# Kernel optimization log

Measured on AMD Instinct MI355X. Metric: run time of the kernel, lower is better.

The kernel has to match this reference:

```python
import jax, jax.numpy as jnp
import numpy as np

T_MAX = 20
NUM_HEADS = 8
COMPLEXITY_W = 0.3
LN_EPS = 1e-5


def _layernorm(h, g, b):
    mu = jnp.mean(h, axis=-1, keepdims=True)
    var = jnp.var(h, axis=-1, keepdims=True)
    return (h - mu) / jnp.sqrt(var + LN_EPS) * g + b


def _gate_mlp(x, W1, b1, g, be, W2, b2, W3, b3):
    # Linear -> LayerNorm -> ReLU -> (Dropout=id in eval) -> Linear -> ReLU -> Linear -> Sigmoid
    h = jax.nn.relu(_layernorm(x @ W1 + b1, g, be))
    h = jax.nn.relu(h @ W2 + b2)
    return jax.nn.sigmoid(h @ W3 + b3)


def _adaptive_windows(x, p):
    S = x.shape[1]
    gate = _gate_mlp(x, p['gW1'], p['gb1'], p['gg'], p['gbe'], p['gW2'], p['gb2'], p['gW3'], p['gb3'])
    comp = _gate_mlp(x, p['cW1'], p['cb1'], p['cg'], p['cbe'], p['cW2'], p['cb2'], p['cW3'], p['cb3'])
    pos = jnp.linspace(0.8, 1.2, S, dtype=x.dtype).reshape(1, -1, 1)
    score = ((1.0 - COMPLEXITY_W) * gate + COMPLEXITY_W * comp) * pos
    T_i = jnp.clip(jnp.ceil(score[..., 0] * T_MAX), 1, T_MAX).astype(jnp.int32)  # [B,S]
    return T_i


def _spike_sum(x, T_i, alpha, beta):
    # LIF recurrence over T_MAX steps; accumulate masked spikes. x: [B,S,E]
    z = jnp.zeros_like(x)

    def step(carry, t):
        v, i, acc = carry
        active = (t < T_i).astype(x.dtype)[..., None]  # [B,S,1]
        i = alpha * i + x * active
        v = beta * v + i
        s = (v >= 1.0).astype(x.dtype)
        v = v * (1.0 - s)  # v_reset = 0
        return (v, i, acc + s * active), None

    (_, _, acc), _ = jax.lax.scan(step, (z, z, z), jnp.arange(T_MAX))
    return acc


def _forward(x, params):
    B, S, E = x.shape
    H, D = NUM_HEADS, E // NUM_HEADS
    q = x @ params['Wq']
    k = x @ params['Wk']
    v = x @ params['Wv']
    T_i = _adaptive_windows(x, params)
    q_sum = _spike_sum(q, T_i, params['alpha_q'], params['beta_q'])
    k_sum = _spike_sum(k, T_i, params['alpha_k'], params['beta_k'])
    v_mean = _spike_sum(v, T_i, params['alpha_v'], params['beta_v']) / T_MAX
    q_sum = q_sum.reshape(B, S, H, D)
    k_sum = k_sum.reshape(B, S, H, D)
    v_mean = v_mean.reshape(B, S, H, D)
    scale = D ** -0.5
    scores = jnp.einsum('bihd,bjhd->bhij', q_sum, k_sum) * scale
    w = jax.nn.softmax(scores, axis=-1)
    out = jnp.einsum('bhij,bjhd->bihd', w, v_mean).reshape(B, S, E)
    return out @ params['Wo'] + params['bo']


def setup_inputs() -> dict:
    key = jax.random.key(0)
    ks = iter(jax.random.split(key, 32))
    B, S, E = 4, 1024, 512
    f32 = jnp.float32

    def w(shape, scale=0.02):
        return jax.random.normal(next(ks), shape, dtype=f32) * scale

    inp = {
        'x': jax.random.normal(next(ks), (B, S, E), dtype=f32),
        'Wq': w((E, E)), 'Wk': w((E, E)), 'Wv': w((E, E)),
        'Wo': w((E, E)), 'bo': jnp.zeros((E,), f32),
        'gW1': w((E, 128)), 'gb1': jnp.zeros((128,), f32),
        'gg': jnp.ones((128,), f32), 'gbe': jnp.zeros((128,), f32),
        'gW2': w((128, 64)), 'gb2': jnp.zeros((64,), f32),
        'gW3': w((64, 1)), 'gb3': jnp.zeros((1,), f32),
        'cW1': w((E, 64)), 'cb1': jnp.zeros((64,), f32),
        'cg': jnp.ones((64,), f32), 'cbe': jnp.zeros((64,), f32),
        'cW2': w((64, 32)), 'cb2': jnp.zeros((32,), f32),
        'cW3': w((32, 1)), 'cb3': jnp.zeros((1,), f32),
        'alpha_q': jnp.asarray(np.exp(-1 / 5.0), f32), 'beta_q': jnp.asarray(np.exp(-1 / 20.0), f32),
        'alpha_k': jnp.asarray(np.exp(-1 / 5.0), f32), 'beta_k': jnp.asarray(np.exp(-1 / 20.0), f32),
        'alpha_v': jnp.asarray(np.exp(-1 / 5.0), f32), 'beta_v': jnp.asarray(np.exp(-1 / 20.0), f32),
    }
    return inp


def reference(x, Wq, Wk, Wv, Wo, bo,
              gW1, gb1, gg, gbe, gW2, gb2, gW3, gb3,
              cW1, cb1, cg, cbe, cW2, cb2, cW3, cb3,
              alpha_q, beta_q, alpha_k, beta_k, alpha_v, beta_v):
    params = dict(Wq=Wq, Wk=Wk, Wv=Wv, Wo=Wo, bo=bo,
                  gW1=gW1, gb1=gb1, gg=gg, gbe=gbe, gW2=gW2, gb2=gb2, gW3=gW3, gb3=gb3,
                  cW1=cW1, cb1=cb1, cg=cg, cbe=cbe, cW2=cW2, cb2=cb2, cW3=cW3, cb3=cb3,
                  alpha_q=alpha_q, beta_q=beta_q, alpha_k=alpha_k, beta_k=beta_k,
                  alpha_v=alpha_v, beta_v=beta_v)
    return _forward(x, params)
```

## Files before the change

### kernel.cpp

```cpp
#include <hip/hip_runtime.h>
#include <math.h>

#define SEQ   1024
#define EMB   512
#define NROWS 4096
#define LDP   72
#define GROWS 4

typedef __attribute__((ext_vector_type(8))) short short8;
typedef __attribute__((ext_vector_type(4))) float float4v;

__device__ __forceinline__ float bf2f(unsigned short s) {
    union { float f; unsigned u; } x; x.u = ((unsigned)s) << 16; return x.f;
}
__device__ __forceinline__ unsigned short f2bf(float f) {
    union { float f; unsigned u; } x; x.f = f;
    unsigned r = x.u + 0x7fffu + ((x.u >> 16) & 1u);
    return (unsigned short)(r >> 16);
}

__device__ __forceinline__ void gld16(const unsigned short* g, short* l) {
    __builtin_amdgcn_global_load_lds(
        (__attribute__((address_space(1))) void*)(g),
        (__attribute__((address_space(3))) void*)(l), 16, 0, 0);
}

__device__ __forceinline__ void split3(float x, unsigned short& h, unsigned short& m, unsigned short& l) {
    union { float f; unsigned u; } a; a.f = x;
    const unsigned rh = a.u + 0x7fffu + ((a.u >> 16) & 1u);
    h = (unsigned short)(rh >> 16);
    union { float f; unsigned u; } hf; hf.u = rh & 0xffff0000u;
    const float r1 = x - hf.f;
    a.f = r1;
    const unsigned rm = a.u + 0x7fffu + ((a.u >> 16) & 1u);
    m = (unsigned short)(rm >> 16);
    union { float f; unsigned u; } mf; mf.u = rm & 0xffff0000u;
    const float r2 = r1 - mf.f;
    l = f2bf(r2);
}

template<int H1, int H2>
__device__ __forceinline__ double mlp_eval(
    const double xs[GROWS][EMB], double* h1, double* h2, double* red,
    double* mu_s, double* var_s,
    const float* __restrict__ W1, const float* __restrict__ b1,
    const float* __restrict__ gam, const float* __restrict__ bet,
    const float* __restrict__ W2, const float* __restrict__ b2,
    const float* __restrict__ W3, const float* __restrict__ b3,
    int tid, int myrow)
{
    constexpr int S  = 256 / H1;
    constexpr int KS = EMB / S;

    {
        const int col = tid % H1, sk = tid / H1;
        double acc[GROWS] = {0.0, 0.0, 0.0, 0.0};
        const int kbeg = sk * KS;
        #pragma unroll 4
        for (int k = kbeg; k < kbeg + KS; ++k) {
            const double w = (double)W1[k * H1 + col];
            #pragma unroll
            for (int r = 0; r < GROWS; ++r) acc[r] += w * xs[r][k];
        }
        #pragma unroll
        for (int r = 0; r < GROWS; ++r) red[(sk * GROWS + r) * H1 + col] = acc[r];
    }
    __syncthreads();
    for (int idx = tid; idx < GROWS * H1; idx += 256) {
        const int r = idx / H1, cc = idx % H1;
        double s = 0.0;
        #pragma unroll
        for (int t = 0; t < S; ++t) s += red[(t * GROWS + r) * H1 + cc];
        h1[r * H1 + cc] = s + (double)b1[cc];
    }
    __syncthreads();

    {
        const int w = tid >> 6, l = tid & 63;
        double s = 0.0;
        for (int c = l; c < H1; c += 64) s += h1[w * H1 + c];
        #pragma unroll
        for (int off = 32; off >= 1; off >>= 1) s += __shfl_xor(s, off);
        if (l == 0) mu_s[w] = s / (double)H1;
    }
    __syncthreads();
    {
        const int w = tid >> 6, l = tid & 63;
        const double mu = mu_s[w];
        double s = 0.0;
        for (int c = l; c < H1; c += 64) { const double d = h1[w * H1 + c] - mu; s += d * d; }
        #pragma unroll
        for (int off = 32; off >= 1; off >>= 1) s += __shfl_xor(s, off);
        if (l == 0) var_s[w] = s / (double)H1;
    }
    __syncthreads();
    for (int idx = tid; idx < GROWS * H1; idx += 256) {
        const int r = idx / H1, cc = idx % H1;
        double hn = (h1[r * H1 + cc] - mu_s[r]) / sqrt(var_s[r] + 1e-5) * (double)gam[cc] + (double)bet[cc];
        h1[r * H1 + cc] = hn > 0.0 ? hn : 0.0;
    }
    __syncthreads();

    {
        const int col = tid % H2;
        const int r   = tid / H2;
        if (r < GROWS) {
            double acc = (double)b2[col];
            for (int k = 0; k < H1; ++k)
                acc += (double)W2[k * H2 + col] * h1[r * H1 + k];
            h2[r * H2 + col] = acc > 0.0 ? acc : 0.0;
        }
    }
    __syncthreads();

    {
        const int w = tid >> 6, l = tid & 63;
        double s = 0.0;
        for (int c = l; c < H2; c += 64) s += h2[w * H2 + c] * (double)W3[c];
        #pragma unroll
        for (int off = 32; off >= 1; off >>= 1) s += __shfl_xor(s, off);
        if (l == 0) mu_s[w] = s;
    }
    __syncthreads();
    double ret = 0.0;
    if (myrow >= 0) {
        const double z = mu_s[myrow] + (double)b3[0];
        ret = 1.0 / (1.0 + exp(-z));
    }
    return ret;
}

__global__ __launch_bounds__(256) void pre_kernel(
    const float* __restrict__ x,
    const float* __restrict__ gW1, const float* __restrict__ gb1,
    const float* __restrict__ gg,  const float* __restrict__ gbe,
    const float* __restrict__ gW2, const float* __restrict__ gb2,
    const float* __restrict__ gW3, const float* __restrict__ gb3,
    const float* __restrict__ cW1, const float* __restrict__ cb1,
    const float* __restrict__ cg,  const float* __restrict__ cbe,
    const float* __restrict__ cW2, const float* __restrict__ cb2,
    const float* __restrict__ cW3, const float* __restrict__ cb3,
    double* __restrict__ scores,
    const float* __restrict__ Wq, const float* __restrict__ Wk,
    const float* __restrict__ Wv, unsigned short* __restrict__ WL,
    unsigned short* __restrict__ XL,
    const float* __restrict__ Wo, unsigned short* __restrict__ WoT)
{
    __shared__ __align__(16) char smem[30784];
    const int bid = blockIdx.x;
    const int tid = threadIdx.x;

    if (bid < 2048) {
        double (*xs)[EMB] = (double(*)[EMB])smem;
        double* h1    = (double*)(smem + 16384);
        double* h2    = (double*)(smem + 20480);
        double* red   = (double*)(smem + 22528);
        double* mu_s  = (double*)(smem + 30720);
        double* var_s = (double*)(smem + 30752);

        const int gx = bid & 1023, gy = bid >> 10;
        const int row0 = gx * GROWS;

        for (int idx = tid; idx < GROWS * EMB; idx += 256) {
            const int r = idx >> 9, cc = idx & 511;
            xs[r][cc] = (double)x[(size_t)(row0 + r) * EMB + cc];
        }
        __syncthreads();

        const int myrow = (tid < GROWS) ? tid : -1;
        double v;
        if (gy == 0)
            v = mlp_eval<128, 64>(xs, h1, h2, red, mu_s, var_s,
                                  gW1, gb1, gg, gbe, gW2, gb2, gW3, gb3, tid, myrow);
        else
            v = mlp_eval<64, 32>(xs, h1, h2, red, mu_s, var_s,
                                 cW1, cb1, cg, cbe, cW2, cb2, cW3, cb3, tid, myrow);

        if (myrow >= 0)
            scores[(size_t)gy * NROWS + row0 + myrow] = v;

    } else if (bid < 3072) {
        unsigned short* Xh = XL;
        unsigned short* Xm = XL + (size_t)NROWS * EMB;
        unsigned short* Xl = Xm + (size_t)NROWS * EMB;
        const size_t i0 = ((size_t)(bid - 2048) * 256 + tid) * 8;
        const float4 a0 = *(const float4*)&x[i0];
        const float4 a1 = *(const float4*)&x[i0 + 4];
        const float av8[8] = {a0.x, a0.y, a0.z, a0.w, a1.x, a1.y, a1.z, a1.w};
        short8 ph, pm, pl;
        #pragma unroll
        for (int e = 0; e < 8; ++e) {
            unsigned short h, m, l;
            split3(av8[e], h, m, l);
            ph[e] = (short)h; pm[e] = (short)m; pl[e] = (short)l;
        }
        *(short8*)&Xh[i0] = ph;
        *(short8*)&Xm[i0] = pm;
        *(short8*)&Xl[i0] = pl;

    } else if (bid < 3264) {
        const int t = bid - 3072;
        const int z = t >> 6, rem = t & 63;
        const int k0 = (rem >> 3) * 64, n0 = (rem & 7) * 64;
        const float* __restrict__ W = (z == 0) ? Wq : (z == 1) ? Wk : Wv;
        unsigned short* Th = WL + (size_t)z * 3 * EMB * EMB;
        unsigned short* Tm = Th + (size_t)EMB * EMB;
        unsigned short* Tl = Tm + (size_t)EMB * EMB;

        float (*Ws)[68] = (float(*)[68])smem;
        #pragma unroll
        for (int it = 0; it < 4; ++it) {
            const int idx = it * 256 + tid;
            const int r = idx >> 4, c4 = (idx & 15) * 4;
            *(float4*)&Ws[r][c4] = *(const float4*)&W[(size_t)(k0 + r) * EMB + n0 + c4];
        }
        __syncthreads();
        #pragma unroll
        for (int it = 0; it < 2; ++it) {
            const int idx = it * 256 + tid;
            const int n = idx >> 3, k8 = (idx & 7) * 8;
            short8 ph, pm, pl;
            #pragma unroll
            for (int j = 0; j < 8; ++j) {
                unsigned short h, m, l;
                split3(Ws[k8 + j][n], h, m, l);
                ph[j] = (short)h; pm[j] = (short)m; pl[j] = (short)l;
            }
            const size_t o = (size_t)(n0 + n) * EMB + k0 + k8;
            *(short8*)&Th[o] = ph;
            *(short8*)&Tm[o] = pm;
            *(short8*)&Tl[o] = pl;
        }

    } else {
        const int t = bid - 3264;
        const int k0 = (t >> 3) * 64, n0 = (t & 7) * 64;
        unsigned short (*Ws)[72] = (unsigned short(*)[72])smem;
        #pragma unroll
        for (int it = 0; it < 4; ++it) {
            const int idx = it * 256 + tid;
            const int r = idx >> 4, c4 = (idx & 15) * 4;
            const float4 w4 = *(const float4*)&Wo[(size_t)(k0 + r) * EMB + n0 + c4];
            Ws[r][c4 + 0] = f2bf(w4.x); Ws[r][c4 + 1] = f2bf(w4.y);
            Ws[r][c4 + 2] = f2bf(w4.z); Ws[r][c4 + 3] = f2bf(w4.w);
        }
        __syncthreads();
        #pragma unroll
        for (int it = 0; it < 2; ++it) {
            const int idx = it * 256 + tid;
            const int n = idx >> 3, k8 = (idx & 7) * 8;
            short8 pack;
            #pragma unroll
            for (int j = 0; j < 8; ++j) pack[j] = (short)Ws[k8 + j][n];
            *(short8*)&WoT[(size_t)(n0 + n) * EMB + k0 + k8] = pack;
        }
    }
}

__global__ __launch_bounds__(256) void qkv_mfma_lif_kernel(
    const unsigned short* __restrict__ XL, const unsigned short* __restrict__ WL,
    const float* __restrict__ aq, const float* __restrict__ bq,
    const float* __restrict__ akp, const float* __restrict__ bkp,
    const float* __restrict__ av, const float* __restrict__ bv,
    const double* __restrict__ scores,
    unsigned short* __restrict__ q_sum, unsigned short* __restrict__ k_sum,
    unsigned short* __restrict__ v_mean)
{
    const int z = blockIdx.z;
    const unsigned short* __restrict__ WTh = WL + (size_t)z * 3 * EMB * EMB;
    const unsigned short* __restrict__ WTm = WTh + (size_t)EMB * EMB;
    const unsigned short* __restrict__ WTl = WTm + (size_t)EMB * EMB;
    const unsigned short* __restrict__ Xh = XL;
    const unsigned short* __restrict__ Xm = XL + (size_t)NROWS * EMB;
    const unsigned short* __restrict__ Xl = Xm + (size_t)NROWS * EMB;
    unsigned short* __restrict__ out = (z == 0) ? q_sum : (z == 1) ? k_sum : v_mean;
    const double alpha = (double)((z == 0) ? aq : (z == 1) ? akp : av)[0];
    const double beta  = (double)((z == 0) ? bq : (z == 1) ? bkp : bv)[0];

    const int phys = blockIdx.x + 8 * blockIdx.y;
    const int logical = (phys & 7) * 32 + (phys >> 3);
    const int bx = logical & 7, by = logical >> 3;
    const int row0 = by * 128, col0 = bx * 64;

    __shared__ __align__(16) short As[3][4096];
    __shared__ __align__(16) short Bs[3][2048];

    const int tid  = threadIdx.x;
    const int lane = tid & 63, wave = tid >> 6;
    const int qd = lane >> 4, c = lane & 15;
    const int wrow = wave * 32;

    const int kc8 = ((lane & 3) ^ ((lane >> 3) & 3)) * 8;
    const size_t ga0 = (size_t)(row0 + wave * 16 + (lane >> 2)) * EMB + kc8;
    const size_t ga1 = ga0 + (size_t)64 * EMB;
    const size_t gb  = (size_t)(col0 + wave * 16 + (lane >> 2)) * EMB + kc8;

    int arf[2], brf[4];
    #pragma unroll
    for (int i = 0; i < 2; ++i) {
        const int Ra = wrow + i * 16 + c;
        arf[i] = Ra * 32 + ((qd ^ ((Ra >> 1) & 3)) * 8);
    }
    #pragma unroll
    for (int j = 0; j < 4; ++j) {
        const int Rb = j * 16 + c;
        brf[j] = Rb * 32 + ((qd ^ ((Rb >> 1) & 3)) * 8);
    }

    float4v acc[2][4];
    #pragma unroll
    for (int i = 0; i < 2; ++i)
        #pragma unroll
        for (int j = 0; j < 4; ++j)
            acc[i][j] = (float4v){0.f, 0.f, 0.f, 0.f};

    for (int k0 = 0; k0 < EMB; k0 += 32) {
        __syncthreads();
        gld16(Xh  + ga0 + k0, &As[0][wave * 512]);
        gld16(Xh  + ga1 + k0, &As[0][2048 + wave * 512]);
        gld16(Xm  + ga0 + k0, &As[1][wave * 512]);
        gld16(Xm  + ga1 + k0, &As[1][2048 + wave * 512]);
        gld16(Xl  + ga0 + k0, &As[2][wave * 512]);
        gld16(Xl  + ga1 + k0, &As[2][2048 + wave * 512]);
        gld16(WTh + gb  + k0, &Bs[0][wave * 512]);
        gld16(WTm + gb  + k0, &Bs[1][wave * 512]);
        gld16(WTl + gb  + k0, &Bs[2][wave * 512]);
        __syncthreads();

        short8 Afh[2], Afm[2], Afl[2];
        #pragma unroll
        for (int i = 0; i < 2; ++i) {
            Afh[i] = *(const short8*)&As[0][arf[i]];
            Afm[i] = *(const short8*)&As[1][arf[i]];
            Afl[i] = *(const short8*)&As[2][arf[i]];
        }
        short8 Bfh[4], Bfm[4], Bfl[4];
        #pragma unroll
        for (int j = 0; j < 4; ++j) {
            Bfh[j] = *(const short8*)&Bs[0][brf[j]];
            Bfm[j] = *(const short8*)&Bs[1][brf[j]];
            Bfl[j] = *(const short8*)&Bs[2][brf[j]];
        }

        #pragma unroll
        for (int i = 0; i < 2; ++i)
            #pragma unroll
            for (int j = 0; j < 4; ++j) {
                float4v t = acc[i][j];
                t = __builtin_amdgcn_mfma_f32_16x16x32_bf16(Afh[i], Bfh[j], t, 0, 0, 0);
                t = __builtin_amdgcn_mfma_f32_16x16x32_bf16(Afh[i], Bfm[j], t, 0, 0, 0);
                t = __builtin_amdgcn_mfma_f32_16x16x32_bf16(Afm[i], Bfh[j], t, 0, 0, 0);
                t = __builtin_amdgcn_mfma_f32_16x16x32_bf16(Afm[i], Bfm[j], t, 0, 0, 0);
                t = __builtin_amdgcn_mfma_f32_16x16x32_bf16(Afh[i], Bfl[j], t, 0, 0, 0);
                t = __builtin_amdgcn_mfma_f32_16x16x32_bf16(Afl[i], Bfh[j], t, 0, 0, 0);
                acc[i][j] = t;
            }
    }

    #pragma unroll
    for (int i = 0; i < 2; ++i)
        #pragma unroll
        for (int r = 0; r < 4; ++r) {
            const int gm = row0 + wrow + i * 16 + qd * 4 + r;
            const double g0 = scores[gm];
            const double c0 = scores[NROWS + gm];
            const int s = gm & (SEQ - 1);
            const double step = (1.2 - 0.8) / (double)(SEQ - 1);
            const double pos  = (double)s * step + 0.8;
            const double score = ((1.0 - 0.3) * g0 + 0.3 * c0) * pos;
            double td = ceil(score * 20.0);
            td = td < 1.0 ? 1.0 : (td > 20.0 ? 20.0 : td);
            const int T = (int)td;
            double cur0 = 0.0, cur1 = 0.0, cur2 = 0.0, cur3 = 0.0;
            double vm0 = 0.0, vm1 = 0.0, vm2 = 0.0, vm3 = 0.0;
            double sp0 = 0.0, sp1 = 0.0, sp2 = 0.0, sp3 = 0.0;
            const double xv0 = (double)acc[i][0][r];
            const double xv1 = (double)acc[i][1][r];
            const double xv2 = (double)acc[i][2][r];
            const double xv3 = (double)acc[i][3][r];
            for (int t = 0; t < T; ++t) {
                cur0 = alpha * cur0 + xv0; vm0 = beta * vm0 + cur0;
                if (vm0 >= 1.0) { sp0 += 1.0; vm0 = 0.0; }
                cur1 = alpha * cur1 + xv1; vm1 = beta * vm1 + cur1;
                if (vm1 >= 1.0) { sp1 += 1.0; vm1 = 0.0; }
                cur2 = alpha * cur2 + xv2; vm2 = beta * vm2 + cur2;
                if (vm2 >= 1.0) { sp2 += 1.0; vm2 = 0.0; }
                cur3 = alpha * cur3 + xv3; vm3 = beta * vm3 + cur3;
                if (vm3 >= 1.0) { sp3 += 1.0; vm3 = 0.0; }
            }
            if (z == 2) { sp0 /= 20.0; sp1 /= 20.0; sp2 /= 20.0; sp3 /= 20.0; }
            const size_t ob = (size_t)gm * EMB + col0 + c;
            out[ob +  0] = f2bf((float)sp0);
            out[ob + 16] = f2bf((float)sp1);
            out[ob + 32] = f2bf((float)sp2);
            out[ob + 48] = f2bf((float)sp3);
        }
}

__global__ __launch_bounds__(256) void attn_mfma_kernel(
    const unsigned short* __restrict__ q, const unsigned short* __restrict__ k,
    const unsigned short* __restrict__ v, unsigned short* __restrict__ attn_bf)
{
    __shared__ __align__(16) short Ks2[2][64 * LDP];
    __shared__ __align__(16) short Vt2[2][64 * LDP];
    __shared__ __align__(16) short Pt[64 * LDP];

    const int b = blockIdx.z, h = blockIdx.y;
    const int i0 = blockIdx.x * 64;
    const int tid  = threadIdx.x;
    const int wave = tid >> 6, lane = tid & 63;
    const int quad = lane >> 4, c = lane & 15;

    const unsigned short* Qb = q + ((size_t)b * SEQ + i0) * EMB + h * 64;
    const unsigned short* Kb = k + (size_t)b * SEQ * EMB + h * 64;
    const unsigned short* Vb = v + (size_t)b * SEQ * EMB + h * 64;

    short8 qf[2];
    {
        const int qrow = wave * 16 + c;
        #pragma unroll
        for (int ks = 0; ks < 2; ++ks) {
            short8 raw = *(const short8*)(Qb + (size_t)qrow * EMB + ks * 32 + quad * 8);
            short8 sc8;
            #pragma unroll
            for (int j = 0; j < 8; ++j)
                sc8[j] = (short)f2bf(bf2f((unsigned short)raw[j]) * 0.125f);
            qf[ks] = sc8;
        }
    }

    const int krow = tid >> 3, kch = tid & 7;
    const int vm_  = tid & 7,  vrp = tid >> 3;
    const int vr   = vrp * 2;
    const int vrch = vr >> 3, vrlow = vr & 7;

    short8 kr0, kr1, vv0, vv1;
    kr0 = *(const short8*)(Kb + (size_t)krow * EMB + kch * 8);
    kr1 = *(const short8*)(Kb + (size_t)(32 + krow) * EMB + kch * 8);
    vv0 = *(const short8*)(Vb + (size_t)vr * EMB + vm_ * 8);
    vv1 = *(const short8*)(Vb + (size_t)(vr + 1) * EMB + vm_ * 8);
    {
        *(short8*)&Ks2[0][krow * LDP + kch * 8] = kr0;
        *(short8*)&Ks2[0][(32 + krow) * LDP + kch * 8] = kr1;
        #pragma unroll
        for (int i = 0; i < 8; ++i) {
            const int d = vm_ * 8 + i;
            const int col = ((vrch ^ vm_) << 3) + vrlow;
            *(int*)&Vt2[0][d * LDP + col] =
                (int)((unsigned)(unsigned short)vv0[i] |
                      ((unsigned)(unsigned short)vv1[i] << 16));
        }
    }

    float m_r[4], l_r[4];
    float4v o[4];
    #pragma unroll
    for (int r = 0; r < 4; ++r) { m_r[r] = -1e30f; l_r[r] = 0.f; }
    #pragma unroll
    for (int nb = 0; nb < 4; ++nb)
        #pragma unroll
        for (int r = 0; r < 4; ++r) o[nb][r] = 0.f;

    for (int jt = 0; jt < SEQ / 64; ++jt) {
        __syncthreads();
        const short* Ks = &Ks2[jt & 1][0];
        const short* Vt = &Vt2[jt & 1][0];

        if (jt + 1 < SEQ / 64) {
            const size_t kb = (size_t)((jt + 1) * 64);
            kr0 = *(const short8*)(Kb + (kb + krow) * EMB + kch * 8);
            kr1 = *(const short8*)(Kb + (kb + 32 + krow) * EMB + kch * 8);
            vv0 = *(const short8*)(Vb + (kb + vr) * EMB + vm_ * 8);
            vv1 = *(const short8*)(Vb + (kb + vr + 1) * EMB + vm_ * 8);
        }

        float sc[4][4];
        #pragma unroll
        for (int nb = 0; nb < 4; ++nb) {
            float4v acc = {0.f, 0.f, 0.f, 0.f};
            #pragma unroll
            for (int ks = 0; ks < 2; ++ks) {
                short8 bfrag = *(const short8*)&Ks[(nb * 16 + c) * LDP + ks * 32 + quad * 8];
                acc = __builtin_amdgcn_mfma_f32_16x16x32_bf16(qf[ks], bfrag, acc, 0, 0, 0);
            }
            #pragma unroll
            for (int r = 0; r < 4; ++r) sc[nb][r] = acc[r];
        }

        float mnew[4], alpha[4];
        #pragma unroll
        for (int r = 0; r < 4; ++r) {
            float mx = fmaxf(fmaxf(sc[0][r], sc[1][r]), fmaxf(sc[2][r], sc[3][r]));
            #pragma unroll
            for (int off = 8; off >= 1; off >>= 1) mx = fmaxf(mx, __shfl_xor(mx, off));
            mnew[r]  = fmaxf(m_r[r], mx);
            alpha[r] = __expf(m_r[r] - mnew[r]);
            m_r[r]   = mnew[r];
        }
        float psum[4] = {0.f, 0.f, 0.f, 0.f};
        #pragma unroll
        for (int nb = 0; nb < 4; ++nb)
            #pragma unroll
            for (int r = 0; r < 4; ++r) {
                float p = __expf(sc[nb][r] - mnew[r]);
                psum[r] += p;
                Pt[(wave * 16 + quad * 4 + r) * LDP + nb * 16 + c] = (short)f2bf(p);
            }
        #pragma unroll
        for (int r = 0; r < 4; ++r) {
            float s = psum[r];
            #pragma unroll
            for (int off = 8; off >= 1; off >>= 1) s += __shfl_xor(s, off);
            l_r[r] = l_r[r] * alpha[r] + s;
            #pragma unroll
            for (int nb = 0; nb < 4; ++nb) o[nb][r] *= alpha[r];
        }

        short8 pf[2];
        #pragma unroll
        for (int ks = 0; ks < 2; ++ks)
            pf[ks] = *(const short8*)&Pt[(wave * 16 + c) * LDP + ks * 32 + quad * 8];
        #pragma unroll
        for (int nb = 0; nb < 4; ++nb) {
            float4v acc = o[nb];
            #pragma unroll
            for (int ks = 0; ks < 2; ++ks) {
                const int d = nb * 16 + c;
                const int kch2 = ks * 4 + quad;
                const int col = ((kch2 ^ (d >> 3)) << 3);
                short8 vfrag = *(const short8*)&Vt[d * LDP + col];
                acc = __builtin_amdgcn_mfma_f32_16x16x32_bf16(pf[ks], vfrag, acc, 0, 0, 0);
            }
            o[nb] = acc;
        }

        if (jt + 1 < SEQ / 64) {
            const int nb2 = (jt + 1) & 1;
            *(short8*)&Ks2[nb2][krow * LDP + kch * 8] = kr0;
            *(short8*)&Ks2[nb2][(32 + krow) * LDP + kch * 8] = kr1;
            #pragma unroll
            for (int i = 0; i < 8; ++i) {
                const int d = vm_ * 8 + i;
                const int col = ((vrch ^ vm_) << 3) + vrlow;
                *(int*)&Vt2[nb2][d * LDP + col] =
                    (int)((unsigned)(unsigned short)vv0[i] |
                          ((unsigned)(unsigned short)vv1[i] << 16));
            }
        }
    }

    #pragma unroll
    for (int r = 0; r < 4; ++r) {
        const float inv = 1.0f / l_r[r];
        const int row = i0 + wave * 16 + quad * 4 + r;
        #pragma unroll
        for (int nb = 0; nb < 4; ++nb)
            attn_bf[((size_t)b * SEQ + row) * EMB + h * 64 + nb * 16 + c] =
                f2bf(o[nb][r] * inv);
    }
}

__global__ __launch_bounds__(256) void out_gemm_kernel(
    const unsigned short* __restrict__ A,
    const unsigned short* __restrict__ BT,
    const float* __restrict__ bias, float* __restrict__ out)
{
    __shared__ __align__(16) short As2[2][4096], Bs2[2][4096];

    const int tid  = threadIdx.x;
    const int lane = tid & 63, wave = tid >> 6;
    const int qd = lane >> 4, c = lane & 15;

    const int phys = blockIdx.x + 8 * blockIdx.y;
    const int logical = (phys & 7) * 64 + (phys >> 3);
    const int bx = logical & 7, by = logical >> 3;
    const int row0 = by * 64, col0 = bx * 64;

    const int sr = tid >> 2, sj = (tid & 3) * 2;
    const size_t gA = (size_t)(row0 + sr) * EMB + sj * 8;
    const size_t gB = (size_t)(col0 + sr) * EMB + sj * 8;
    const int dA0 = sr * 64 + ((sj ^ (sr & 7)) * 8);
    const int dA1 = sr * 64 + (((sj + 1) ^ (sr & 7)) * 8);

    int arf[2], brf[4][2];
    #pragma unroll
    for (int kk = 0; kk < 2; ++kk) {
        arf[kk] = (wave * 16 + c) * 64 + (((kk * 4 + qd) ^ (c & 7)) * 8);
        #pragma unroll
        for (int j = 0; j < 4; ++j)
            brf[j][kk] = (j * 16 + c) * 64 + (((kk * 4 + qd) ^ (c & 7)) * 8);
    }

    float4v acc[4];
    #pragma unroll
    for (int j = 0; j < 4; ++j) acc[j] = (float4v){0.f, 0.f, 0.f, 0.f};

    short8 ra0, ra1, rb0, rb1;
    ra0 = *(const short8*)&A[gA];      ra1 = *(const short8*)&A[gA + 8];
    rb0 = *(const short8*)&BT[gB];     rb1 = *(const short8*)&BT[gB + 8];
    *(short8*)&As2[0][dA0] = ra0; *(short8*)&As2[0][dA1] = ra1;
    *(short8*)&Bs2[0][dA0] = rb0; *(short8*)&Bs2[0][dA1] = rb1;

    for (int it = 0; it < 8; ++it) {
        __syncthreads();
        const int cur = it & 1;
        if (it < 7) {
            const int k0 = (it + 1) * 64;
            ra0 = *(const short8*)&A[gA + k0];  ra1 = *(const short8*)&A[gA + k0 + 8];
            rb0 = *(const short8*)&BT[gB + k0]; rb1 = *(const short8*)&BT[gB + k0 + 8];
        }
        #pragma unroll
        for (int kk = 0; kk < 2; ++kk) {
            const short8 af = *(const short8*)&As2[cur][arf[kk]];
            #pragma unroll
            for (int j = 0; j < 4; ++j) {
                const short8 bf = *(const short8*)&Bs2[cur][brf[j][kk]];
                acc[j] = __builtin_amdgcn_mfma_f32_16x16x32_bf16(af, bf, acc[j], 0, 0, 0);
            }
        }
        if (it < 7) {
            const int nxt = cur ^ 1;
            *(short8*)&As2[nxt][dA0] = ra0; *(short8*)&As2[nxt][dA1] = ra1;
            *(short8*)&Bs2[nxt][dA0] = rb0; *(short8*)&Bs2[nxt][dA1] = rb1;
        }
    }

    #pragma unroll
    for (int j = 0; j < 4; ++j)
        #pragma unroll
        for (int r = 0; r < 4; ++r) {
            const int gm = row0 + wave * 16 + qd * 4 + r;
            const int gn = col0 + j * 16 + c;
            out[(size_t)gm * EMB + gn] = acc[j][r] + bias[gn];
        }
}

extern "C" void kernel_launch(void* const* d_in, const int* in_sizes, int n_in,
                              void* d_out, int out_size, void* d_ws, size_t ws_size,
                              hipStream_t stream)
{
    const float* x   = (const float*)d_in[0];
    const float* Wq  = (const float*)d_in[1];
    const float* Wk  = (const float*)d_in[2];
    const float* Wv  = (const float*)d_in[3];
    const float* Wo  = (const float*)d_in[4];
    const float* bo  = (const float*)d_in[5];
    const float* gW1 = (const float*)d_in[6];
    const float* gb1 = (const float*)d_in[7];
    const float* gg  = (const float*)d_in[8];
    const float* gbe = (const float*)d_in[9];
    const float* gW2 = (const float*)d_in[10];
    const float* gb2 = (const float*)d_in[11];
    const float* gW3 = (const float*)d_in[12];
    const float* gb3 = (const float*)d_in[13];
    const float* cW1 = (const float*)d_in[14];
    const float* cb1 = (const float*)d_in[15];
    const float* cg  = (const float*)d_in[16];
    const float* cbe = (const float*)d_in[17];
    const float* cW2 = (const float*)d_in[18];
    const float* cb2 = (const float*)d_in[19];
    const float* cW3 = (const float*)d_in[20];
    const float* cb3 = (const float*)d_in[21];
    const float* aq  = (const float*)d_in[22];
    const float* bq  = (const float*)d_in[23];
    const float* ak  = (const float*)d_in[24];
    const float* bk  = (const float*)d_in[25];
    const float* av  = (const float*)d_in[26];
    const float* bv  = (const float*)d_in[27];

    unsigned short* q_sum   = (unsigned short*)((char*)d_ws + 16384);
    unsigned short* k_sum   = q_sum   + (size_t)NROWS * EMB;
    unsigned short* v_mean  = k_sum   + (size_t)NROWS * EMB;
    unsigned short* attn_bf = v_mean  + (size_t)NROWS * EMB;
    unsigned short* WoT     = attn_bf + (size_t)NROWS * EMB;
    unsigned short* WL      = WoT     + (size_t)EMB * EMB;
    unsigned short* XLp     = WL      + (size_t)9 * EMB * EMB;
    double* scores          = (double*)(XLp + (size_t)3 * NROWS * EMB);
    float* out = (float*)d_out;

    pre_kernel<<<dim3(3328), dim3(256), 0, stream>>>(
        x, gW1, gb1, gg, gbe, gW2, gb2, gW3, gb3,
        cW1, cb1, cg, cbe, cW2, cb2, cW3, cb3, scores,
        Wq, Wk, Wv, WL, XLp, Wo, WoT);

    qkv_mfma_lif_kernel<<<dim3(EMB / 64, NROWS / 128, 3), dim3(256), 0, stream>>>(
        XLp, WL, aq, bq, ak, bk, av, bv, scores, q_sum, k_sum, v_mean);

    attn_mfma_kernel<<<dim3(SEQ / 64, 8, 4), dim3(256), 0, stream>>>(
        q_sum, k_sum, v_mean, attn_bf);

    out_gemm_kernel<<<dim3(EMB / 64, NROWS / 64), dim3(256), 0, stream>>>(
        attn_bf, WoT, bo, out);
}
```

Measured before the change: 248.3 us.

## Split-K the output GEMM and store gate-MLP input tile as float

The output projection GEMM is split along K into two halves over a z grid dimension. One half writes into the output and the other into a workspace buffer, and a new elementwise kernel adds the two together with the bias. Separately, the gate/complexity MLP blocks now stage x in shared memory as float using float4 copies instead of converting to double, which halves that buffer and the LDS footprint. The split-K doubles the GEMM block count to improve occupancy, at the cost of an extra kernel launch and an extra read/write pass over the full output tensor.

Result: slower. 265.7 us (+7.0%).

```diff
diff --git a/kernel.cpp b/kernel.cpp
--- a/kernel.cpp
+++ b/kernel.cpp
@@ -41,7 +41,7 @@
 
 template<int H1, int H2>
 __device__ __forceinline__ double mlp_eval(
-    const double xs[GROWS][EMB], double* h1, double* h2, double* red,
+    const float xs[GROWS][EMB], double* h1, double* h2, double* red,
     double* mu_s, double* var_s,
     const float* __restrict__ W1, const float* __restrict__ b1,
     const float* __restrict__ gam, const float* __restrict__ bet,
@@ -60,7 +60,7 @@
         for (int k = kbeg; k < kbeg + KS; ++k) {
             const double w = (double)W1[k * H1 + col];
             #pragma unroll
-            for (int r = 0; r < GROWS; ++r) acc[r] += w * xs[r][k];
+            for (int r = 0; r < GROWS; ++r) acc[r] += w * (double)xs[r][k];
         }
         #pragma unroll
         for (int r = 0; r < GROWS; ++r) red[(sk * GROWS + r) * H1 + col] = acc[r];
@@ -146,24 +146,26 @@
     unsigned short* __restrict__ XL,
     const float* __restrict__ Wo, unsigned short* __restrict__ WoT)
 {
-    __shared__ __align__(16) char smem[30784];
+    __shared__ __align__(16) char smem[22592];
     const int bid = blockIdx.x;
     const int tid = threadIdx.x;
 
     if (bid < 2048) {
-        double (*xs)[EMB] = (double(*)[EMB])smem;
-        double* h1    = (double*)(smem + 16384);
-        double* h2    = (double*)(smem + 20480);
-        double* red   = (double*)(smem + 22528);
-        double* mu_s  = (double*)(smem + 30720);
-        double* var_s = (double*)(smem + 30752);
+        float (*xs)[EMB] = (float(*)[EMB])smem;
+        double* h1    = (double*)(smem + 8192);
+        double* h2    = (double*)(smem + 12288);
+        double* red   = (double*)(smem + 14336);
+        double* mu_s  = (double*)(smem + 22528);
+        double* var_s = (double*)(smem + 22560);
 
         const int gx = bid & 1023, gy = bid >> 10;
         const int row0 = gx * GROWS;
 
-        for (int idx = tid; idx < GROWS * EMB; idx += 256) {
-            const int r = idx >> 9, cc = idx & 511;
-            xs[r][cc] = (double)x[(size_t)(row0 + r) * EMB + cc];
+        {
+            const float4* src = (const float4*)&x[(size_t)row0 * EMB];
+            float4* dst = (float4*)smem;
+            for (int idx = tid; idx < GROWS * EMB / 4; idx += 256)
+                dst[idx] = src[idx];
         }
         __syncthreads();
 
@@ -563,13 +565,15 @@
 __global__ __launch_bounds__(256) void out_gemm_kernel(
     const unsigned short* __restrict__ A,
     const unsigned short* __restrict__ BT,
-    const float* __restrict__ bias, float* __restrict__ out)
+    float* __restrict__ out, float* __restrict__ p1)
 {
     __shared__ __align__(16) short As2[2][4096], Bs2[2][4096];
 
     const int tid  = threadIdx.x;
     const int lane = tid & 63, wave = tid >> 6;
     const int qd = lane >> 4, c = lane & 15;
+    const int zk = blockIdx.z;
+    const int kbase = zk * 256;
 
     const int phys = blockIdx.x + 8 * blockIdx.y;
     const int logical = (phys & 7) * 64 + (phys >> 3);
@@ -577,8 +581,8 @@
     const int row0 = by * 64, col0 = bx * 64;
 
     const int sr = tid >> 2, sj = (tid & 3) * 2;
-    const size_t gA = (size_t)(row0 + sr) * EMB + sj * 8;
-    const size_t gB = (size_t)(col0 + sr) * EMB + sj * 8;
+    const size_t gA = (size_t)(row0 + sr) * EMB + sj * 8 + kbase;
+    const size_t gB = (size_t)(col0 + sr) * EMB + sj * 8 + kbase;
     const int dA0 = sr * 64 + ((sj ^ (sr & 7)) * 8);
     const int dA1 = sr * 64 + (((sj + 1) ^ (sr & 7)) * 8);
 
@@ -601,10 +605,10 @@
     *(short8*)&As2[0][dA0] = ra0; *(short8*)&As2[0][dA1] = ra1;
     *(short8*)&Bs2[0][dA0] = rb0; *(short8*)&Bs2[0][dA1] = rb1;
 
-    for (int it = 0; it < 8; ++it) {
+    for (int it = 0; it < 4; ++it) {
         __syncthreads();
         const int cur = it & 1;
-        if (it < 7) {
+        if (it < 3) {
             const int k0 = (it + 1) * 64;
             ra0 = *(const short8*)&A[gA + k0];  ra1 = *(const short8*)&A[gA + k0 + 8];
             rb0 = *(const short8*)&BT[gB + k0]; rb1 = *(const short8*)&BT[gB + k0 + 8];
@@ -618,21 +622,36 @@
                 acc[j] = __builtin_amdgcn_mfma_f32_16x16x32_bf16(af, bf, acc[j], 0, 0, 0);
             }
         }
-        if (it < 7) {
+        if (it < 3) {
             const int nxt = cur ^ 1;
             *(short8*)&As2[nxt][dA0] = ra0; *(short8*)&As2[nxt][dA1] = ra1;
             *(short8*)&Bs2[nxt][dA0] = rb0; *(short8*)&Bs2[nxt][dA1] = rb1;
         }
     }
 
+    float* __restrict__ dst = (zk == 0) ? out : p1;
     #pragma unroll
     for (int j = 0; j < 4; ++j)
         #pragma unroll
         for (int r = 0; r < 4; ++r) {
             const int gm = row0 + wave * 16 + qd * 4 + r;
             const int gn = col0 + j * 16 + c;
-            out[(size_t)gm * EMB + gn] = acc[j][r] + bias[gn];
-        }
+            dst[(size_t)gm * EMB + gn] = acc[j][r];
+        }
+}
+
+__global__ __launch_bounds__(256) void out_combine_kernel(
+    float* __restrict__ out, const float* __restrict__ p1,
+    const float* __restrict__ bias)
+{
+    const size_t i0 = ((size_t)blockIdx.x * 256 + threadIdx.x) * 4;
+    float4 a = *(const float4*)&out[i0];
+    const float4 b = *(const float4*)&p1[i0];
+    const int col = (int)(i0 & (EMB - 1));
+    const float4 bb = *(const float4*)&bias[col];
+    a.x += b.x + bb.x; a.y += b.y + bb.y;
+    a.z += b.z + bb.z; a.w += b.w + bb.w;
+    *(float4*)&out[i0] = a;
 }
 
 extern "C" void kernel_launch(void* const* d_in, const int* in_sizes, int n_in,
@@ -676,6 +695,7 @@
     unsigned short* WL      = WoT     + (size_t)EMB * EMB;
     unsigned short* XLp     = WL      + (size_t)9 * EMB * EMB;
     double* scores          = (double*)(XLp + (size_t)3 * NROWS * EMB);
+    float* p1               = (float*)(scores + 2 * NROWS);
     float* out = (float*)d_out;
 
     pre_kernel<<<dim3(3328), dim3(256), 0, stream>>>(
@@ -689,6 +709,9 @@
     attn_mfma_kernel<<<dim3(SEQ / 64, 8, 4), dim3(256), 0, stream>>>(
         q_sum, k_sum, v_mean, attn_bf);
 
-    out_gemm_kernel<<<dim3(EMB / 64, NROWS / 64), dim3(256), 0, stream>>>(
-        attn_bf, WoT, bo, out);
-}
+    out_gemm_kernel<<<dim3(EMB / 64, NROWS / 64, 2), dim3(256), 0, stream>>>(
+        attn_bf, WoT, out, p1);
+
+    out_combine_kernel<<<dim3(NROWS * EMB / (256 * 4)), dim3(256), 0, stream>>>(
+        out, p1, bo);
+}
```
